# Kernel optimization log

Hardware: AMD Instinct MI355X
Metric: run time of the kernel (lower is better)

Reference implementation:

```python
import jax, jax.numpy as jnp
import numpy as np
import math

B, T, D = 2, 2048, 2048
N_HEADS, N_KV, HEAD_DIM = 16, 4, 128
INTER = 8192
MAX_POS = 4096
ROPE_BASE = 10000.0
EPS = 1e-6


def _rope_tables():
    inv_freq = 1.0 / (ROPE_BASE ** (jnp.arange(0, HEAD_DIM, 2, dtype=jnp.float32) / HEAD_DIM))
    t = jnp.arange(MAX_POS, dtype=jnp.float32)
    freqs = jnp.einsum('i,j->ij', t, inv_freq)          # [MAX_POS, HEAD_DIM//2]
    emb = jnp.concatenate([freqs, freqs], axis=-1)      # [MAX_POS, HEAD_DIM]
    return jnp.cos(emb), jnp.sin(emb)


def _apply_rope(x, cos, sin):
    # x: [B,H,T,Dh]; cos/sin: [B,T,Dh] (gathered by position_ids)
    c = cos[:, None, :, :]
    s = sin[:, None, :, :]
    x1 = x[..., ::2]
    x2 = x[..., 1::2]
    x_rot = jnp.stack([-x2, x1], axis=-1).reshape(x.shape)  # interleave(-x2, x1)
    return x * c + x_rot * s


def _rms_norm(x, w):
    var = jnp.mean(x * x, axis=-1, keepdims=True)
    return w * (x * jax.lax.rsqrt(var + EPS))


def setup_inputs() -> dict:
    key = jax.random.key(0)
    ks = jax.random.split(key, 10)
    s = 0.02
    hidden_states = jax.random.normal(ks[0], (B, T, D), dtype=jnp.float32)
    # additive causal mask
    causal = jnp.tril(jnp.ones((T, T), dtype=bool))
    attention_mask = jnp.where(causal, 0.0, -1e9).astype(jnp.float32)[None, None]
    position_ids = jnp.arange(B * T).reshape(B, T)  # values < MAX_POS
    return {
        'hidden_states': hidden_states,
        'attention_mask': attention_mask,
        'position_ids': position_ids,
        'attn_norm_w': jnp.ones((D,), jnp.float32),
        'mlp_norm_w': jnp.ones((D,), jnp.float32),
        'wq': jax.random.normal(ks[1], (D, N_HEADS * HEAD_DIM), jnp.float32) * s,
        'wk': jax.random.normal(ks[2], (D, N_KV * HEAD_DIM), jnp.float32) * s,
        'wv': jax.random.normal(ks[3], (D, N_KV * HEAD_DIM), jnp.float32) * s,
        'wo': jax.random.normal(ks[4], (N_HEADS * HEAD_DIM, D), jnp.float32) * s,
        'gate_w': jax.random.normal(ks[5], (D, D), jnp.float32) * s,
        'gate_b': jnp.zeros((D,), jnp.float32),
        'fc1_w': jax.random.normal(ks[6], (D, INTER), jnp.float32) * s,
        'fc2_w': jax.random.normal(ks[7], (INTER, D), jnp.float32) * s,
    }


def reference(hidden_states, attention_mask, position_ids, attn_norm_w, mlp_norm_w,
              wq, wk, wv, wo, gate_w, gate_b, fc1_w, fc2_w):
    b, t, _ = hidden_states.shape
    residual = hidden_states
    h = _rms_norm(hidden_states, attn_norm_w)

    # elementwise sigmoid output gate: [B,T,D] -> [B,H,T,Dh]
    gate = jax.nn.sigmoid(h @ gate_w + gate_b)
    gate = gate.reshape(b, t, N_HEADS, HEAD_DIM).transpose(0, 2, 1, 3)

    q = (h @ wq).reshape(b, t, N_HEADS, HEAD_DIM).transpose(0, 2, 1, 3)
    k = (h @ wk).reshape(b, t, N_KV, HEAD_DIM).transpose(0, 2, 1, 3)
    v = (h @ wv).reshape(b, t, N_KV, HEAD_DIM).transpose(0, 2, 1, 3)

    cos_t, sin_t = _rope_tables()
    cos = cos_t[position_ids]  # [B,T,Dh]
    sin = sin_t[position_ids]
    q = _apply_rope(q, cos, sin)
    k = _apply_rope(k, cos, sin)

    n_rep = N_HEADS // N_KV
    k = jnp.repeat(k, n_rep, axis=1)  # GQA expand to [B,H,T,Dh]
    v = jnp.repeat(v, n_rep, axis=1)

    scores = jnp.einsum('bhqd,bhkd->bhqk', q, k) / math.sqrt(HEAD_DIM)
    scores = scores + attention_mask
    attn = jax.nn.softmax(scores, axis=-1)
    out = jnp.einsum('bhqk,bhkd->bhqd', attn, v) * gate
    out = out.transpose(0, 2, 1, 3).reshape(b, t, N_HEADS * HEAD_DIM) @ wo

    h = residual + out
    residual = h
    h2 = _rms_norm(h, mlp_norm_w)
    mlp_out = jax.nn.silu(h2 @ fc1_w) @ fc2_w
    return residual + mlp_out
```

## Files before the change

kernel.cpp:

```cpp
#include <hip/hip_runtime.h>
#include <hip/hip_bf16.h>
#include <cstdint>
#include <cstddef>

#define BB 2
#define TT 2048
#define DD 2048
#define NH 16
#define NKV 4
#define HD 128
#define NI 8192
#define MM (BB*TT)

typedef __bf16 bf16x8 __attribute__((ext_vector_type(8)));
typedef float  f32x4  __attribute__((ext_vector_type(4)));

__device__ __forceinline__ void gload_lds16(const void* g, void* l) {
  __builtin_amdgcn_global_load_lds((__attribute__((address_space(1))) void*)g,
                                   (__attribute__((address_space(3))) void*)l,
                                   16, 0, 0);
}

__device__ __forceinline__ int xcd_swizzle(int wg, int nwg) {
  int xcd = wg & 7;
  int l = wg >> 3;
  int q = nwg >> 3, r = nwg & 7;
  return (xcd < r ? xcd * (q + 1) : r * (q + 1) + (xcd - r) * q) + l;
}

__global__ __launch_bounds__(128) void rope_tables_k(float* __restrict__ cosT,
                                                     float* __restrict__ sinT) {
  int pos = blockIdx.x;
  int d = threadIdx.x;
  int f = d & 63;
  float inv = powf(10000.0f, -((float)(2 * f)) / 128.0f);
  float ang = inv * (float)pos;
  cosT[pos * 128 + d] = cosf(ang);
  sinT[pos * 128 + d] = sinf(ang);
}

template <typename TIN>
__global__ __launch_bounds__(256) void transpose_to_bf16_k(const TIN* __restrict__ in,
                                                           __bf16* __restrict__ out,
                                                           int R, int C) {
  __shared__ float t[32][33];
  int c0 = blockIdx.x * 32, r0 = blockIdx.y * 32;
  int tx = threadIdx.x & 31;
  int ty = threadIdx.x >> 5;
#pragma unroll
  for (int i = 0; i < 4; i++) {
    int r = ty + i * 8;
    t[r][tx] = (float)in[(size_t)(r0 + r) * C + c0 + tx];
  }
  __syncthreads();
#pragma unroll
  for (int i = 0; i < 4; i++) {
    int r = ty + i * 8;
    out[(size_t)(c0 + r) * R + r0 + tx] = (__bf16)t[tx][r];
  }
}

__global__ __launch_bounds__(256) void rmsnorm_k(const float* __restrict__ x,
                                                 const float* __restrict__ w,
                                                 __bf16* __restrict__ out) {
  int row = blockIdx.x;
  const float* xr = x + (size_t)row * DD;
  int t = threadIdx.x;
  float4 a = ((const float4*)xr)[2 * t];
  float4 b = ((const float4*)xr)[2 * t + 1];
  float ss = a.x * a.x + a.y * a.y + a.z * a.z + a.w * a.w +
             b.x * b.x + b.y * b.y + b.z * b.z + b.w * b.w;
#pragma unroll
  for (int off = 32; off; off >>= 1) ss += __shfl_xor(ss, off, 64);
  __shared__ float red[4];
  if ((t & 63) == 0) red[t >> 6] = ss;
  __syncthreads();
  float tot = red[0] + red[1] + red[2] + red[3];
  float rs = rsqrtf(tot * (1.0f / DD) + 1e-6f);
  const float4 w1 = ((const float4*)w)[2 * t];
  const float4 w2 = ((const float4*)w)[2 * t + 1];
  bf16x8 ov;
  ov[0] = (__bf16)(a.x * rs * w1.x);
  ov[1] = (__bf16)(a.y * rs * w1.y);
  ov[2] = (__bf16)(a.z * rs * w1.z);
  ov[3] = (__bf16)(a.w * rs * w1.w);
  ov[4] = (__bf16)(b.x * rs * w2.x);
  ov[5] = (__bf16)(b.y * rs * w2.y);
  ov[6] = (__bf16)(b.z * rs * w2.z);
  ov[7] = (__bf16)(b.w * rs * w2.w);
  *(bf16x8*)(out + (size_t)row * DD + t * 8) = ov;
}

enum { G_QG = 0, G_RES = 1, G_SILU = 2, G_PART = 3 };

template <int EPI>
__global__ __launch_bounds__(512) void gemm256_k(
    const __bf16* __restrict__ A, const __bf16* __restrict__ Bt,
    __bf16* __restrict__ outB, float* __restrict__ outF,
    __bf16* __restrict__ outQ, __bf16* __restrict__ outG,
    const float* __restrict__ bias, const float* __restrict__ residual,
    const float* __restrict__ cosT, const float* __restrict__ sinT,
    const int* __restrict__ posids, int N, int K, int ldk, float oscale) {
  __shared__ __align__(16) __bf16 Ab[3][256 * 32];
  __shared__ __align__(16) __bf16 Bb[3][256 * 32];
  const int tid = threadIdx.x;
  const int lane = tid & 63;
  const int wid = tid >> 6;
  const int wr = wid >> 2;
  const int wc = wid & 3;
  const int fr = lane & 15;
  const int fg = lane >> 4;

  const int nwg = gridDim.x * gridDim.y;
  int wg = xcd_swizzle(blockIdx.y * gridDim.x + blockIdx.x, nwg);
  const int bx = wg % gridDim.x, by = wg / gridDim.x;
  const int m0 = by * 256;
  const int n0 = bx * 256;
  const int kz = blockIdx.z;
  const int kBase = kz * K;

  const int srow0 = wid * 32 + (lane >> 2);
  const int scol = (((lane & 3) ^ ((lane >> 3) & 3)) << 3);
  const __bf16* aS0 = A + (size_t)(m0 + srow0) * ldk + kBase + scol;
  const __bf16* aS1 = aS0 + (size_t)16 * ldk;
  const __bf16* bS0 = Bt + (size_t)(n0 + srow0) * ldk + kBase + scol;
  const __bf16* bS1 = bS0 + (size_t)16 * ldk;
  const int e0 = (wid * 2) * 512;
  const int e1 = (wid * 2 + 1) * 512;

  const int nt = K / 32;

#define STAGE256(kt, s)                             \
  {                                                 \
    const int k0_ = (kt) * 32;                      \
    gload_lds16(aS0 + k0_, &Ab[(s)][e0]);           \
    gload_lds16(aS1 + k0_, &Ab[(s)][e1]);           \
    gload_lds16(bS0 + k0_, &Bb[(s)][e0]);           \
    gload_lds16(bS1 + k0_, &Bb[(s)][e1]);           \
  }

  STAGE256(0, 0);
  if (nt > 1) STAGE256(1, 1);
  asm volatile("s_waitcnt vmcnt(4)" ::: "memory");
  __builtin_amdgcn_s_barrier();
  __builtin_amdgcn_sched_barrier(0);

  f32x4 acc[8][4];
#pragma unroll
  for (int i = 0; i < 8; i++)
#pragma unroll
    for (int j = 0; j < 4; j++) acc[i][j] = (f32x4){0.f, 0.f, 0.f, 0.f};

  const int asl = (fg ^ ((fr >> 1) & 3)) * 8;

  for (int t = 0; t < nt; ++t) {
    const int s = t % 3;
    if (t + 2 < nt) STAGE256(t + 2, (t + 2) % 3);
    bf16x8 af[8], bfr[4];
#pragma unroll
    for (int mi = 0; mi < 8; mi++)
      af[mi] = *(const bf16x8*)&Ab[s][(wr * 128 + mi * 16 + fr) * 32 + asl];
#pragma unroll
    for (int ni = 0; ni < 4; ni++)
      bfr[ni] = *(const bf16x8*)&Bb[s][(wc * 64 + ni * 16 + fr) * 32 + asl];
    __builtin_amdgcn_s_setprio(1);
#pragma unroll
    for (int mi = 0; mi < 8; mi++)
#pragma unroll
      for (int ni = 0; ni < 4; ni++)
        acc[mi][ni] =
            __builtin_amdgcn_mfma_f32_16x16x32_bf16(af[mi], bfr[ni], acc[mi][ni], 0, 0, 0);
    __builtin_amdgcn_s_setprio(0);
    if (t + 1 < nt) {
      if (t + 2 < nt) {
        asm volatile("s_waitcnt vmcnt(4)" ::: "memory");
      } else {
        asm volatile("s_waitcnt vmcnt(0)" ::: "memory");
      }
      __builtin_amdgcn_s_barrier();
      __builtin_amdgcn_sched_barrier(0);
    }
  }
#undef STAGE256

#pragma unroll
  for (int mi = 0; mi < 8; mi++) {
    const int row = m0 + wr * 128 + mi * 16 + fg * 4;
#pragma unroll
    for (int ni = 0; ni < 4; ni++) {
      const int col = n0 + wc * 64 + ni * 16 + fr;
#pragma unroll
      for (int j = 0; j < 4; j++) {
        float v = acc[mi][ni][j];
        const int r = row + j;
        if constexpr (EPI == G_QG) {
          float vp = __shfl_xor(v, 1, 64);
          if (n0 < 2048) {
            int pos = posids[r];
            int d = col & 127;
            float c = cosT[pos * 128 + d], sn = sinT[pos * 128 + d];
            float o = (col & 1) ? (v * c + vp * sn) : (v * c - vp * sn);
            outQ[(size_t)r * 2048 + col] = (__bf16)(o * oscale);
          } else {
            float xx = v + bias[col - 2048];
            outG[(size_t)r * 2048 + (col - 2048)] = (__bf16)(1.0f / (1.0f + expf(-xx)));
          }
        } else if constexpr (EPI == G_RES) {
          outF[(size_t)r * N + col] = v + residual[(size_t)r * N + col];
        } else if constexpr (EPI == G_SILU) {
          outB[(size_t)r * N + col] = (__bf16)(v / (1.0f + expf(-v)));
        } else {
          outB[(size_t)(kz * MM + r) * N + col] = (__bf16)v;
        }
      }
    }
  }
}

__global__ __launch_bounds__(256) void combine_k(const __bf16* __restrict__ parts,
                                                 const float* __restrict__ h1,
                                                 float* __restrict__ out) {
  size_t i = ((size_t)blockIdx.x * 256 + threadIdx.x) * 8;
  bf16x8 p0 = *(const bf16x8*)&parts[i];
  bf16x8 p1 = *(const bf16x8*)&parts[(size_t)MM * 2048 + i];
  float4 a = *(const float4*)&h1[i];
  float4 b = *(const float4*)&h1[i + 4];
  float4 o0, o1;
  o0.x = (float)p0[0] + (float)p1[0] + a.x;
  o0.y = (float)p0[1] + (float)p1[1] + a.y;
  o0.z = (float)p0[2] + (float)p1[2] + a.z;
  o0.w = (float)p0[3] + (float)p1[3] + a.w;
  o1.x = (float)p0[4] + (float)p1[4] + b.x;
  o1.y = (float)p0[5] + (float)p1[5] + b.y;
  o1.z = (float)p0[6] + (float)p1[6] + b.z;
  o1.w = (float)p0[7] + (float)p1[7] + b.w;
  *(float4*)&out[i] = o0;
  *(float4*)&out[i + 4] = o1;
}

__global__ __launch_bounds__(256) void gemm_kv_k(
    const __bf16* __restrict__ A, const __bf16* __restrict__ Bt,
    __bf16* __restrict__ kOut, __bf16* __restrict__ vOut,
    const float* __restrict__ cosT, const float* __restrict__ sinT,
    const int* __restrict__ posids, int K) {
  __shared__ __align__(16) __bf16 As[128 * 32];
  __shared__ __align__(16) __bf16 Bs[128 * 32];
  const int tid = threadIdx.x;
  const int lane = tid & 63;
  const int w = tid >> 6;
  const int wm = w >> 1, wn = w & 1;

  const int nwg = gridDim.x * gridDim.y;
  int wg = xcd_swizzle(blockIdx.y * gridDim.x + blockIdx.x, nwg);
  const int bx = wg % gridDim.x, by = wg / gridDim.x;
  const int m0 = by * 128;
  const int n0 = bx * 128;

  const int lr = lane >> 2;
  const int lc = (lane & 3) * 8;
  const __bf16* aSrc = A + (size_t)(m0 + 32 * w + lr) * K + lc;
  const __bf16* bSrc = Bt + (size_t)(n0 + 32 * w + lr) * K + lc;
  __bf16* aDst = &As[w * 1024];
  __bf16* bDst = &Bs[w * 1024];

  f32x4 acc[4][4];
#pragma unroll
  for (int i = 0; i < 4; i++)
#pragma unroll
    for (int j = 0; j < 4; j++) acc[i][j] = (f32x4){0.f, 0.f, 0.f, 0.f};

  const int fr = lane & 15;
  const int fc = (lane >> 4) * 8;

  for (int k0 = 0; k0 < K; k0 += 32) {
    __syncthreads();
    gload_lds16(aSrc + k0, aDst);
    gload_lds16(aSrc + k0 + (size_t)16 * K, aDst + 512);
    gload_lds16(bSrc + k0, bDst);
    gload_lds16(bSrc + k0 + (size_t)16 * K, bDst + 512);
    asm volatile("s_waitcnt vmcnt(0)" ::: "memory");
    __syncthreads();

    bf16x8 af[4], bfg[4];
#pragma unroll
    for (int i = 0; i < 4; i++)
      af[i] = *(const bf16x8*)&As[(wm * 64 + i * 16 + fr) * 32 + fc];
#pragma unroll
    for (int i = 0; i < 4; i++)
      bfg[i] = *(const bf16x8*)&Bs[(wn * 64 + i * 16 + fr) * 32 + fc];
#pragma unroll
    for (int mi = 0; mi < 4; mi++)
#pragma unroll
      for (int ni = 0; ni < 4; ni++)
        acc[mi][ni] =
            __builtin_amdgcn_mfma_f32_16x16x32_bf16(af[mi], bfg[ni], acc[mi][ni], 0, 0, 0);
  }

  const int fg = lane >> 4;
#pragma unroll
  for (int mi = 0; mi < 4; mi++) {
#pragma unroll
    for (int ni = 0; ni < 4; ni++) {
#pragma unroll
      for (int j = 0; j < 4; j++) {
        int row = m0 + wm * 64 + mi * 16 + fg * 4 + j;
        int col = n0 + wn * 64 + ni * 16 + fr;
        float v = acc[mi][ni][j];
        float vp = __shfl_xor(v, 1, 64);
        if (col < 512) {
          int pos = posids[row];
          int d = col & 127;
          float c = cosT[pos * 128 + d];
          float s = sinT[pos * 128 + d];
          float o = (col & 1) ? (v * c + vp * s) : (v * c - vp * s);
          kOut[(size_t)row * 512 + col] = (__bf16)o;
        } else {
          vOut[(size_t)row * 512 + (col - 512)] = (__bf16)v;
        }
      }
    }
  }
}

__global__ __launch_bounds__(256) void attn_k(const __bf16* __restrict__ Q,
                                              const __bf16* __restrict__ Kb,
                                              const __bf16* __restrict__ Vt,
                                              const __bf16* __restrict__ Gate,
                                              __bf16* __restrict__ Out) {
  __shared__ __align__(16) __bf16 Ks[2][64 * 128];
  __shared__ __align__(16) __bf16 Vs[2][128 * 64];
  __shared__ __align__(16) __bf16 Ps[4][16 * 64];
  const int tid = threadIdx.x;
  const int lane = tid & 63;
  const int w = tid >> 6;
  const int fr = lane & 15;
  const int fg = lane >> 4;

  const int nwg = gridDim.x * gridDim.y;
  int wg = xcd_swizzle(blockIdx.y * gridDim.x + blockIdx.x, nwg);
  const int qb = wg % gridDim.x;
  const int bh = wg / gridDim.x;
  const int q0 = qb * 64;
  const int b = bh >> 4, h = bh & 15;
  const int g = h >> 2;

  const size_t qrow = (size_t)(b * TT + q0 + w * 16 + fr);
  bf16x8 qf[4];
#pragma unroll
  for (int kt = 0; kt < 4; kt++)
    qf[kt] = *(const bf16x8*)&Q[qrow * 2048 + h * 128 + kt * 32 + fg * 8];

  const __bf16* kPtr[4];
  const __bf16* vPtr[4];
#pragma unroll
  for (int i = 0; i < 4; i++) {
    int krow = w * 16 + i * 4 + (lane >> 4);
    int kcol8 = (lane & 15) ^ (krow & 15);
    kPtr[i] = Kb + (size_t)(b * TT + krow) * 512 + g * 128 + kcol8 * 8;
    int dloc = w * 32 + i * 8 + (lane >> 3);
    int kv8 = (lane & 7) ^ (dloc & 7);
    vPtr[i] = Vt + (size_t)(g * 128 + dloc) * (size_t)MM + b * TT + kv8 * 8;
  }

  f32x4 o[8];
#pragma unroll
  for (int i = 0; i < 8; i++) o[i] = (f32x4){0.f, 0.f, 0.f, 0.f};
  float mrow[4] = {-3e38f, -3e38f, -3e38f, -3e38f};
  float lrow[4] = {0.f, 0.f, 0.f, 0.f};

  const int nsteps = qb + 1;

#pragma unroll
  for (int i = 0; i < 4; i++) {
    gload_lds16(kPtr[i], &Ks[0][w * 2048 + i * 512]);
    gload_lds16(vPtr[i], &Vs[0][w * 2048 + i * 512]);
  }
  __syncthreads();

  for (int t = 0; t < nsteps; t++) {
    const int cur = t & 1;
    const int kb = t * 64;
    if (t + 1 < nsteps) {
      const int nb = kb + 64;
#pragma unroll
      for (int i = 0; i < 4; i++) {
        gload_lds16(kPtr[i] + (size_t)nb * 512, &Ks[cur ^ 1][w * 2048 + i * 512]);
        gload_lds16(vPtr[i] + nb, &Vs[cur ^ 1][w * 2048 + i * 512]);
      }
    }

    f32x4 s[4];
#pragma unroll
    for (int nc = 0; nc < 4; nc++) s[nc] = (f32x4){0.f, 0.f, 0.f, 0.f};
#pragma unroll
    for (int nc = 0; nc < 4; nc++)
#pragma unroll
      for (int kt = 0; kt < 4; kt++) {
        bf16x8 kf = *(const bf16x8*)&Ks[cur][(nc * 16 + fr) * 128 + (((kt * 4 + fg) ^ fr) << 3)];
        s[nc] = __builtin_amdgcn_mfma_f32_16x16x32_bf16(qf[kt], kf, s[nc], 0, 0, 0);
      }

    float alpha[4];
#pragma unroll
    for (int j = 0; j < 4; j++) {
      const int qr = q0 + w * 16 + fg * 4 + j;
      float pv[4];
#pragma unroll
      for (int nc = 0; nc < 4; nc++) {
        int kc = kb + nc * 16 + fr;
        float val = s[nc][j];
        if (kc > qr) val = -1e9f;
        pv[nc] = val;
      }
      float tmx = fmaxf(fmaxf(pv[0], pv[1]), fmaxf(pv[2], pv[3]));
      tmx = fmaxf(tmx, __shfl_xor(tmx, 1, 64));
      tmx = fmaxf(tmx, __shfl_xor(tmx, 2, 64));
      tmx = fmaxf(tmx, __shfl_xor(tmx, 4, 64));
      tmx = fmaxf(tmx, __shfl_xor(tmx, 8, 64));
      float mnew = fmaxf(mrow[j], tmx);
      alpha[j] = __expf(mrow[j] - mnew);
      mrow[j] = mnew;
      float rsum = 0.f;
      const int q = fg * 4 + j;
#pragma unroll
      for (int nc = 0; nc < 4; nc++) {
        float e = __expf(pv[nc] - mnew);
        rsum += e;
        Ps[w][q * 64 + (((nc * 2 + (fr >> 3)) ^ (q & 7)) << 3) + (fr & 7)] = (__bf16)e;
      }
      rsum += __shfl_xor(rsum, 1, 64);
      rsum += __shfl_xor(rsum, 2, 64);
      rsum += __shfl_xor(rsum, 4, 64);
      rsum += __shfl_xor(rsum, 8, 64);
      lrow[j] = lrow[j] * alpha[j] + rsum;
    }
#pragma unroll
    for (int nd = 0; nd < 8; nd++)
#pragma unroll
      for (int j = 0; j < 4; j++) o[nd][j] *= alpha[j];

    bf16x8 pa[2];
#pragma unroll
    for (int sl = 0; sl < 2; sl++)
      pa[sl] = *(const bf16x8*)&Ps[w][fr * 64 + (((sl * 4 + fg) ^ (fr & 7)) << 3)];
#pragma unroll
    for (int nd = 0; nd < 8; nd++)
#pragma unroll
      for (int sl = 0; sl < 2; sl++) {
        bf16x8 vf =
            *(const bf16x8*)&Vs[cur][(nd * 16 + fr) * 64 + (((sl * 4 + fg) ^ (fr & 7)) << 3)];
        o[nd] = __builtin_amdgcn_mfma_f32_16x16x32_bf16(pa[sl], vf, o[nd], 0, 0, 0);
      }
    __syncthreads();
  }

  float invl[4];
#pragma unroll
  for (int j = 0; j < 4; j++) invl[j] = 1.0f / lrow[j];
#pragma unroll
  for (int nd = 0; nd < 8; nd++) {
#pragma unroll
    for (int j = 0; j < 4; j++) {
      int row = q0 + w * 16 + fg * 4 + j;
      int d = nd * 16 + fr;
      size_t idx = (size_t)(b * TT + row) * 2048 + h * 128 + d;
      float val = o[nd][j] * invl[j] * (float)Gate[idx];
      Out[idx] = (__bf16)val;
    }
  }
}

extern "C" void kernel_launch(void* const* d_in, const int* in_sizes, int n_in,
                              void* d_out, int out_size, void* d_ws, size_t ws_size,
                              hipStream_t stream) {
  const float* hidden = (const float*)d_in[0];
  const int* posids = (const int*)d_in[2];
  const float* attn_w = (const float*)d_in[3];
  const float* mlp_w = (const float*)d_in[4];
  const float* wq = (const float*)d_in[5];
  const float* wk = (const float*)d_in[6];
  const float* wv = (const float*)d_in[7];
  const float* wo = (const float*)d_in[8];
  const float* gw = (const float*)d_in[9];
  const float* gb = (const float*)d_in[10];
  const float* f1 = (const float*)d_in[11];
  const float* f2 = (const float*)d_in[12];

  char* p = (char*)d_ws;
  auto alloc = [&](size_t n) {
    char* r = p;
    p += (n + 255) & ~(size_t)255;
    return r;
  };
  __bf16* wqg_t = (__bf16*)alloc((size_t)4096 * 2048 * 2);
  __bf16* wkv_t = (__bf16*)alloc((size_t)1024 * 2048 * 2);
  __bf16* wo_t = (__bf16*)alloc((size_t)2048 * 2048 * 2);
  __bf16* f1_t = (__bf16*)alloc((size_t)NI * 2048 * 2);
  __bf16* f2_t = (__bf16*)alloc((size_t)2048 * NI * 2);
  __bf16* h_bf = (__bf16*)alloc((size_t)MM * DD * 2);
  float* h1 = (float*)alloc((size_t)MM * 2048 * 4);

  char* regionA = alloc((size_t)64 * 1024 * 1024);
  __bf16* q_bf = (__bf16*)(regionA);
  __bf16* gate_bf = (__bf16*)(regionA + (size_t)16 * 1024 * 1024);
  __bf16* attn_g = (__bf16*)(regionA + (size_t)32 * 1024 * 1024);
  __bf16* k_bf = (__bf16*)(regionA + (size_t)48 * 1024 * 1024);
  __bf16* v_bf = (__bf16*)(regionA + (size_t)52 * 1024 * 1024);
  __bf16* v_t = (__bf16*)(regionA + (size_t)56 * 1024 * 1024);
  float* cosT = (float*)(regionA + (size_t)60 * 1024 * 1024);
  float* sinT = (float*)(regionA + (size_t)62 * 1024 * 1024);
  __bf16* mlp1 = (__bf16*)(regionA);
  __bf16* parts = (__bf16*)f1_t;

  rope_tables_k<<<4096, 128, 0, stream>>>(cosT, sinT);

  transpose_to_bf16_k<float><<<dim3(64, 64), 256, 0, stream>>>(wq, wqg_t, 2048, 2048);
  transpose_to_bf16_k<float><<<dim3(64, 64), 256, 0, stream>>>(gw, wqg_t + (size_t)2048 * 2048, 2048, 2048);
  transpose_to_bf16_k<float><<<dim3(16, 64), 256, 0, stream>>>(wk, wkv_t, 2048, 512);
  transpose_to_bf16_k<float><<<dim3(16, 64), 256, 0, stream>>>(wv, wkv_t + (size_t)512 * 2048, 2048, 512);
  transpose_to_bf16_k<float><<<dim3(64, 64), 256, 0, stream>>>(wo, wo_t, 2048, 2048);
  transpose_to_bf16_k<float><<<dim3(256, 64), 256, 0, stream>>>(f1, f1_t, 2048, NI);
  transpose_to_bf16_k<float><<<dim3(64, 256), 256, 0, stream>>>(f2, f2_t, NI, 2048);

  rmsnorm_k<<<MM, 256, 0, stream>>>(hidden, attn_w, h_bf);

  const float qsc = 0.08838834764831845f;
  gemm256_k<G_QG><<<dim3(16, 16), 512, 0, stream>>>(
      h_bf, wqg_t, nullptr, nullptr, q_bf, gate_bf, gb, nullptr, cosT, sinT, posids,
      4096, 2048, 2048, qsc);
  gemm_kv_k<<<dim3(8, 32), 256, 0, stream>>>(h_bf, wkv_t, k_bf, v_bf, cosT, sinT, posids, 2048);

  transpose_to_bf16_k<__bf16><<<dim3(16, 128), 256, 0, stream>>>(v_bf, v_t, MM, 512);

  attn_k<<<dim3(32, 32), 256, 0, stream>>>(q_bf, k_bf, v_t, gate_bf, attn_g);

  gemm256_k<G_RES><<<dim3(8, 16), 512, 0, stream>>>(
      attn_g, wo_t, nullptr, h1, nullptr, nullptr, nullptr, hidden, nullptr, nullptr, nullptr,
      2048, 2048, 2048, 1.0f);

  rmsnorm_k<<<MM, 256, 0, stream>>>(h1, mlp_w, h_bf);

  gemm256_k<G_SILU><<<dim3(32, 16), 512, 0, stream>>>(
      h_bf, f1_t, mlp1, nullptr, nullptr, nullptr, nullptr, nullptr, nullptr, nullptr, nullptr,
      NI, 2048, 2048, 1.0f);

  gemm256_k<G_PART><<<dim3(8, 16, 2), 512, 0, stream>>>(
      mlp1, f2_t, parts, nullptr, nullptr, nullptr, nullptr, nullptr, nullptr, nullptr, nullptr,
      2048, 4096, NI, 1.0f);

  combine_k<<<4096, 256, 0, stream>>>(parts, h1, (float*)d_out);
}
```

Measured before the change: 904.3 us.

## Split GEMM main loop into two MFMA phases and split-K the Wo projection

```diff
diff --git a/kernel.cpp b/kernel.cpp
--- a/kernel.cpp
+++ b/kernel.cpp
@@ -130,20 +130,25 @@
 
   const int nt = K / 32;
 
-#define STAGE256(kt, s)                             \
-  {                                                 \
-    const int k0_ = (kt) * 32;                      \
-    gload_lds16(aS0 + k0_, &Ab[(s)][e0]);           \
-    gload_lds16(aS1 + k0_, &Ab[(s)][e1]);           \
-    gload_lds16(bS0 + k0_, &Bb[(s)][e0]);           \
-    gload_lds16(bS1 + k0_, &Bb[(s)][e1]);           \
-  }
-
-  STAGE256(0, 0);
-  if (nt > 1) STAGE256(1, 1);
+#define STAGE_A(kt, s)                          \
+  {                                             \
+    const int k0_ = (kt) * 32;                  \
+    gload_lds16(aS0 + k0_, &Ab[(s)][e0]);       \
+    gload_lds16(aS1 + k0_, &Ab[(s)][e1]);       \
+  }
+#define STAGE_B(kt, s)                          \
+  {                                             \
+    const int k0_ = (kt) * 32;                  \
+    gload_lds16(bS0 + k0_, &Bb[(s)][e0]);       \
+    gload_lds16(bS1 + k0_, &Bb[(s)][e1]);       \
+  }
+
+  STAGE_A(0, 0);
+  STAGE_B(0, 0);
+  STAGE_A(1, 1);
+  STAGE_B(1, 1);
   asm volatile("s_waitcnt vmcnt(4)" ::: "memory");
   __builtin_amdgcn_s_barrier();
-  __builtin_amdgcn_sched_barrier(0);
 
   f32x4 acc[8][4];
 #pragma unroll
@@ -155,33 +160,52 @@
 
   for (int t = 0; t < nt; ++t) {
     const int s = t % 3;
-    if (t + 2 < nt) STAGE256(t + 2, (t + 2) % 3);
-    bf16x8 af[8], bfr[4];
-#pragma unroll
-    for (int mi = 0; mi < 8; mi++)
+    const int sn = (t + 2) % 3;
+    bf16x8 af[4], bfr[4];
+#pragma unroll
+    for (int mi = 0; mi < 4; mi++)
       af[mi] = *(const bf16x8*)&Ab[s][(wr * 128 + mi * 16 + fr) * 32 + asl];
 #pragma unroll
     for (int ni = 0; ni < 4; ni++)
       bfr[ni] = *(const bf16x8*)&Bb[s][(wc * 64 + ni * 16 + fr) * 32 + asl];
+    if (t + 2 < nt) STAGE_A(t + 2, sn);
+    __builtin_amdgcn_s_barrier();
+    asm volatile("s_waitcnt lgkmcnt(0)" ::: "memory");
+    __builtin_amdgcn_sched_barrier(0);
     __builtin_amdgcn_s_setprio(1);
 #pragma unroll
-    for (int mi = 0; mi < 8; mi++)
+    for (int mi = 0; mi < 4; mi++)
 #pragma unroll
       for (int ni = 0; ni < 4; ni++)
         acc[mi][ni] =
             __builtin_amdgcn_mfma_f32_16x16x32_bf16(af[mi], bfr[ni], acc[mi][ni], 0, 0, 0);
     __builtin_amdgcn_s_setprio(0);
-    if (t + 1 < nt) {
-      if (t + 2 < nt) {
-        asm volatile("s_waitcnt vmcnt(4)" ::: "memory");
-      } else {
-        asm volatile("s_waitcnt vmcnt(0)" ::: "memory");
-      }
-      __builtin_amdgcn_s_barrier();
-      __builtin_amdgcn_sched_barrier(0);
+    __builtin_amdgcn_s_barrier();
+    bf16x8 af2[4];
+#pragma unroll
+    for (int mi = 0; mi < 4; mi++)
+      af2[mi] = *(const bf16x8*)&Ab[s][(wr * 128 + (mi + 4) * 16 + fr) * 32 + asl];
+    if (t + 2 < nt) {
+      STAGE_B(t + 2, sn);
+      asm volatile("s_waitcnt vmcnt(4)" ::: "memory");
+    } else {
+      asm volatile("s_waitcnt vmcnt(0)" ::: "memory");
     }
-  }
-#undef STAGE256
+    __builtin_amdgcn_s_barrier();
+    asm volatile("s_waitcnt lgkmcnt(0)" ::: "memory");
+    __builtin_amdgcn_sched_barrier(0);
+    __builtin_amdgcn_s_setprio(1);
+#pragma unroll
+    for (int mi = 0; mi < 4; mi++)
+#pragma unroll
+      for (int ni = 0; ni < 4; ni++)
+        acc[mi + 4][ni] =
+            __builtin_amdgcn_mfma_f32_16x16x32_bf16(af2[mi], bfr[ni], acc[mi + 4][ni], 0, 0, 0);
+    __builtin_amdgcn_s_setprio(0);
+    __builtin_amdgcn_s_barrier();
+  }
+#undef STAGE_A
+#undef STAGE_B
 
 #pragma unroll
   for (int mi = 0; mi < 8; mi++) {
@@ -198,8 +222,8 @@
           if (n0 < 2048) {
             int pos = posids[r];
             int d = col & 127;
-            float c = cosT[pos * 128 + d], sn = sinT[pos * 128 + d];
-            float o = (col & 1) ? (v * c + vp * sn) : (v * c - vp * sn);
+            float c = cosT[pos * 128 + d], sn2 = sinT[pos * 128 + d];
+            float o = (col & 1) ? (v * c + vp * sn2) : (v * c - vp * sn2);
             outQ[(size_t)r * 2048 + col] = (__bf16)(o * oscale);
           } else {
             float xx = v + bias[col - 2048];
@@ -218,13 +242,13 @@
 }
 
 __global__ __launch_bounds__(256) void combine_k(const __bf16* __restrict__ parts,
-                                                 const float* __restrict__ h1,
+                                                 const float* __restrict__ res,
                                                  float* __restrict__ out) {
   size_t i = ((size_t)blockIdx.x * 256 + threadIdx.x) * 8;
   bf16x8 p0 = *(const bf16x8*)&parts[i];
   bf16x8 p1 = *(const bf16x8*)&parts[(size_t)MM * 2048 + i];
-  float4 a = *(const float4*)&h1[i];
-  float4 b = *(const float4*)&h1[i + 4];
+  float4 a = *(const float4*)&res[i];
+  float4 b = *(const float4*)&res[i + 4];
   float4 o0, o1;
   o0.x = (float)p0[0] + (float)p1[0] + a.x;
   o0.y = (float)p0[1] + (float)p1[1] + a.y;
@@ -510,7 +534,8 @@
   float* cosT = (float*)(regionA + (size_t)60 * 1024 * 1024);
   float* sinT = (float*)(regionA + (size_t)62 * 1024 * 1024);
   __bf16* mlp1 = (__bf16*)(regionA);
-  __bf16* parts = (__bf16*)f1_t;
+  __bf16* parts_wo = (__bf16*)(regionA);
+  __bf16* parts_fc2 = (__bf16*)f1_t;
 
   rope_tables_k<<<4096, 128, 0, stream>>>(cosT, sinT);
 
@@ -534,9 +559,10 @@
 
   attn_k<<<dim3(32, 32), 256, 0, stream>>>(q_bf, k_bf, v_t, gate_bf, attn_g);
 
-  gemm256_k<G_RES><<<dim3(8, 16), 512, 0, stream>>>(
-      attn_g, wo_t, nullptr, h1, nullptr, nullptr, nullptr, hidden, nullptr, nullptr, nullptr,
-      2048, 2048, 2048, 1.0f);
+  gemm256_k<G_PART><<<dim3(8, 16, 2), 512, 0, stream>>>(
+      attn_g, wo_t, parts_wo, nullptr, nullptr, nullptr, nullptr, nullptr, nullptr, nullptr,
+      nullptr, 2048, 1024, 2048, 1.0f);
+  combine_k<<<4096, 256, 0, stream>>>(parts_wo, hidden, h1);
 
   rmsnorm_k<<<MM, 256, 0, stream>>>(h1, mlp_w, h_bf);
 
@@ -545,8 +571,8 @@
       NI, 2048, 2048, 1.0f);
 
   gemm256_k<G_PART><<<dim3(8, 16, 2), 512, 0, stream>>>(
-      mlp1, f2_t, parts, nullptr, nullptr, nullptr, nullptr, nullptr, nullptr, nullptr, nullptr,
-      2048, 4096, NI, 1.0f);
-
-  combine_k<<<4096, 256, 0, stream>>>(parts, h1, (float*)d_out);
-}
+      mlp1, f2_t, parts_fc2, nullptr, nullptr, nullptr, nullptr, nullptr, nullptr, nullptr,
+      nullptr, 2048, 4096, NI, 1.0f);
+
+  combine_k<<<4096, 256, 0, stream>>>(parts_fc2, h1, (float*)d_out);
+}
```

Result: faster. 792.8 us (-12.3%).
